# Kernel tuning notes

Measured on AMD Instinct MI355X. Metric: run time of the kernel, lower is better.

The kernel has to match this reference:

```python
import jax, jax.numpy as jnp
import numpy as np

N_NODES = 50000
N_EDGES = 800000
IN_DIM = 128
HID = 128
NUM_CLASSES = 2


def setup_inputs() -> dict:
    key = jax.random.key(0)
    ks = jax.random.split(key, 16)
    inp = {
        "adj_row": jax.random.randint(ks[0], (N_EDGES,), 0, N_NODES),
        "adj_col": jax.random.randint(ks[1], (N_EDGES,), 0, N_NODES),
        "adj_vals": jax.random.uniform(ks[2], (N_EDGES,), dtype=jnp.float32),
        "input_feature": jax.random.normal(ks[3], (N_NODES, IN_DIM), dtype=jnp.float32),
        "graph_indicator": jax.random.randint(ks[4], (N_NODES,), 0, 64),
        # GCN layer params (kaiming-uniform-ish init; zeros bias like the torch module)
        "W1": jax.random.uniform(ks[5], (IN_DIM, HID), jnp.float32, -1, 1) * np.sqrt(6.0 / IN_DIM),
        "b1": jnp.zeros((HID,), jnp.float32),
        "W2": jax.random.uniform(ks[6], (HID, HID), jnp.float32, -1, 1) * np.sqrt(6.0 / HID),
        "b2": jnp.zeros((HID,), jnp.float32),
        "W3": jax.random.uniform(ks[7], (HID, HID), jnp.float32, -1, 1) * np.sqrt(6.0 / HID),
        "b3": jnp.zeros((HID,), jnp.float32),
        # fc params (torch.nn.Linear default init range)
        "fcW1": jax.random.uniform(ks[8], (3 * HID, HID), jnp.float32, -1, 1) / np.sqrt(3 * HID),
        "fcb1": jax.random.uniform(ks[9], (HID,), jnp.float32, -1, 1) / np.sqrt(3 * HID),
        "fcW2": jax.random.uniform(ks[10], (HID, HID // 2), jnp.float32, -1, 1) / np.sqrt(HID),
        "fcb2": jax.random.uniform(ks[11], (HID // 2,), jnp.float32, -1, 1) / np.sqrt(HID),
        "fcW3": jax.random.uniform(ks[12], (HID // 2, NUM_CLASSES), jnp.float32, -1, 1) / np.sqrt(HID // 2),
        "fcb3": jax.random.uniform(ks[13], (NUM_CLASSES,), jnp.float32, -1, 1) / np.sqrt(HID // 2),
    }
    return inp


def _gcn_layer(row, col, vals, x, W, b, n_nodes):
    # support = X @ W  -> dense GEMM
    support = x @ W
    # sparse.mm(A, support): out[i] = sum_{e: row[e]=i} vals[e] * support[col[e]]
    msgs = support[col] * vals[:, None]  # [E, D] gather + scale
    agg = jax.ops.segment_sum(msgs, row, num_segments=n_nodes)
    return agg + b


def reference(adj_row, adj_col, adj_vals, input_feature, graph_indicator,
              W1, b1, W2, b2, W3, b3, fcW1, fcb1, fcW2, fcb2, fcW3, fcb3):
    n = input_feature.shape[0]
    g1 = jax.nn.relu(_gcn_layer(adj_row, adj_col, adj_vals, input_feature, W1, b1, n))
    g2 = jax.nn.relu(_gcn_layer(adj_row, adj_col, adj_vals, g1, W2, b2, n))
    g3 = jax.nn.relu(_gcn_layer(adj_row, adj_col, adj_vals, g2, W3, b3, n))
    feat = jnp.concatenate([g1, g2, g3], axis=1)  # [N, 3*HID]
    h = jax.nn.relu(feat @ fcW1 + fcb1)
    h = jax.nn.relu(h @ fcW2 + fcb2)
    logits = h @ fcW3 + fcb3
    return logits
```

## Files before the change

### kernel.cpp

```cpp
#include <hip/hip_runtime.h>
#include <hip/hip_bf16.h>

#define N_NODES 50000
#define N_EDGES 800000
#define NBK 391
#define BCAP 2560
#define PADSLACK 896

static inline int cdiv(int a, int b) { return (a + b - 1) / b; }

typedef __attribute__((ext_vector_type(8))) short short8;
typedef __attribute__((ext_vector_type(4))) float f32x4;

__device__ __forceinline__ float b2f(unsigned short u) {
    union { unsigned int i; float f; } c;
    c.i = ((unsigned int)u) << 16;
    return c.f;
}
__device__ __forceinline__ unsigned short f2bb(float f) {
    __hip_bfloat16 h = __float2bfloat16(f);
    return *(unsigned short*)&h;
}

__device__ __forceinline__ void pack_one(const float* __restrict__ W,
                                         __hip_bfloat16* __restrict__ out,
                                         int K, int N, int t) {
    int lane = t & 63;
    int kc = (t >> 6) % (K / 32);
    int nt = (t >> 6) / (K / 32);
    int kbase = kc * 32 + (lane >> 4) * 8;
    int col = nt * 16 + (lane & 15);
    __hip_bfloat16* dst = out + (size_t)t * 8;
#pragma unroll
    for (int j = 0; j < 8; ++j)
        dst[j] = __float2bfloat16(W[(size_t)(kbase + j) * N + col]);
}

__global__ __launch_bounds__(256)
void stage1_kernel(const int* __restrict__ row, const int* __restrict__ col,
                   const float* __restrict__ vals, int* __restrict__ bcursor,
                   int2* __restrict__ tmp, int E,
                   const float* __restrict__ x, __hip_bfloat16* __restrict__ support,
                   int M,
                   const float* __restrict__ W1, const float* __restrict__ W2,
                   const float* __restrict__ W3, const float* __restrict__ fcW1,
                   const float* __restrict__ fcW2,
                   __hip_bfloat16* __restrict__ pW2, __hip_bfloat16* __restrict__ pW3,
                   __hip_bfloat16* __restrict__ pfcW1, __hip_bfloat16* __restrict__ pfcW2) {
    __shared__ unsigned short As[64][136];
    __shared__ int hist[NBK];
    __shared__ int base[NBK];
    const int b = blockIdx.x;
    const int tid = threadIdx.x;

    if (b < 196) {
        const int CH = 4096;
        int e0 = b * CH;
        for (int i = tid; i < NBK; i += 256) hist[i] = 0;
        __syncthreads();
        for (int i = tid; i < CH; i += 256) {
            int e = e0 + i;
            if (e < E) atomicAdd(&hist[row[e] >> 7], 1);
        }
        __syncthreads();
        for (int i = tid; i < NBK; i += 256) {
            int c = hist[i];
            base[i] = (c > 0) ? (i * BCAP + atomicAdd(&bcursor[i], c)) : 0;
            hist[i] = 0;
        }
        __syncthreads();
        for (int i = tid; i < CH; i += 256) {
            int e = e0 + i;
            if (e < E) {
                int r = row[e];
                int bk = r >> 7;
                int rk = atomicAdd(&hist[bk], 1);
                tmp[base[bk] + rk] = make_int2(((r & 127) << 16) | col[e],
                                               __float_as_int(vals[e]));
            }
        }
        return;
    }

    if (b < 978) {
        const int wave = tid >> 6;
        const int lane = tid & 63;
        const int ln15 = lane & 15;
        const int quad = lane >> 4;
        const int m0 = (b - 196) * 64;

        short8 bfr[4][2];
#pragma unroll
        for (int kc = 0; kc < 4; ++kc)
#pragma unroll
            for (int h = 0; h < 2; ++h)
#pragma unroll
                for (int j = 0; j < 8; ++j)
                    bfr[kc][h][j] = (short)f2bb(
                        W1[(size_t)(kc * 32 + quad * 8 + j) * 128 + (wave * 2 + h) * 16 + ln15]);

#pragma unroll
        for (int i = 0; i < 4; ++i) {
            int idx = tid + i * 256;
            int r = idx >> 4;
            int c8 = (idx & 15) * 8;
            uint4 pk = {0, 0, 0, 0};
            if (m0 + r < M) {
                const float* src = &x[(size_t)(m0 + r) * 128 + c8];
                float4 a = *(const float4*)src;
                float4 bq = *(const float4*)(src + 4);
                pk.x = f2bb(a.x) | ((unsigned int)f2bb(a.y) << 16);
                pk.y = f2bb(a.z) | ((unsigned int)f2bb(a.w) << 16);
                pk.z = f2bb(bq.x) | ((unsigned int)f2bb(bq.y) << 16);
                pk.w = f2bb(bq.z) | ((unsigned int)f2bb(bq.w) << 16);
            }
            *(uint4*)&As[r][c8] = pk;
        }
        __syncthreads();

        f32x4 acc[4][2];
#pragma unroll
        for (int s = 0; s < 4; ++s)
#pragma unroll
            for (int h = 0; h < 2; ++h) acc[s][h] = (f32x4){0.f, 0.f, 0.f, 0.f};
#pragma unroll
        for (int kc = 0; kc < 4; ++kc) {
            short8 af[4];
#pragma unroll
            for (int s = 0; s < 4; ++s)
                af[s] = *(const short8*)&As[s * 16 + ln15][kc * 32 + quad * 8];
#pragma unroll
            for (int s = 0; s < 4; ++s)
#pragma unroll
                for (int h = 0; h < 2; ++h)
                    acc[s][h] = __builtin_amdgcn_mfma_f32_16x16x32_bf16(
                        af[s], bfr[kc][h], acc[s][h], 0, 0, 0);
        }
#pragma unroll
        for (int s = 0; s < 4; ++s)
#pragma unroll
            for (int h = 0; h < 2; ++h) {
                int cl = (wave * 2 + h) * 16 + ln15;
#pragma unroll
                for (int r = 0; r < 4; ++r) {
                    int rw = m0 + s * 16 + quad * 4 + r;
                    if (rw < M)
                        support[(size_t)rw * 128 + cl] = __float2bfloat16(acc[s][h][r]);
                }
            }
        return;
    }

    int pb = b - 978;
    if (pb < 8)       pack_one(W2,  pW2,  128, 128, pb * 256 + tid);
    else if (pb < 16) pack_one(W3,  pW3,  128, 128, (pb - 8) * 256 + tid);
    else if (pb < 40) pack_one(fcW1, pfcW1, 384, 128, (pb - 16) * 256 + tid);
    else              pack_one(fcW2, pfcW2, 128, 64, (pb - 40) * 256 + tid);
}

__global__ __launch_bounds__(256)
void binB_kernel(const int2* __restrict__ tmp, const int* __restrict__ bcursor,
                 int2* __restrict__ rowrange, int2* __restrict__ epack, int N) {
    int b = blockIdx.x;
    int r0 = b << 7;
    int nr = N - r0; if (nr > 128) nr = 128;
    __shared__ int cnt[128];
    __shared__ int cur[128];
    __shared__ int rpos[128];
    __shared__ int red[256];
    int t = threadIdx.x;
    int partial = 0;
    for (int i = t; i < b; i += 256) partial += bcursor[i];
    red[t] = partial;
    if (t < 128) cnt[t] = 0;
    __syncthreads();
    for (int off = 128; off > 0; off >>= 1) {
        if (t < off) red[t] += red[t + off];
        __syncthreads();
    }
    int slab = b * BCAP;
    int send = slab + bcursor[b];
    for (int i = slab + t; i < send; i += 256)
        atomicAdd(&cnt[tmp[i].x >> 16], 1);
    __syncthreads();
    int rcnt = (t < 128) ? cnt[t] : 0;
    int pc = (rcnt + 7) & ~7;
    if (t < 128) cur[t] = pc;
    __syncthreads();
    for (int off = 1; off < 128; off <<= 1) {
        int u = (t >= off && t < 128) ? cur[t - off] : 0;
        __syncthreads();
        if (t < 128) cur[t] += u;
        __syncthreads();
    }
    int obase = red[0] + b * PADSLACK;
    if (t < 128) {
        int pos = obase + cur[t] - pc;
        rpos[t] = pos;
        cur[t] = pos;
        if (t < nr) rowrange[r0 + t] = make_int2(pos, pos + pc);
    }
    __syncthreads();
    for (int i = slab + t; i < send; i += 256) {
        int2 v = tmp[i];
        int rl = v.x >> 16;
        int c = v.x & 0xffff;
        int pos = atomicAdd(&cur[rl], 1);
        epack[pos] = make_int2(c, v.y);
    }
    if (t < 128) {
        int rc = rcnt;
        int pos = rpos[t];
#pragma unroll 1
        for (int i = pos + rc; i < pos + pc; ++i)
            epack[i] = make_int2(0, 0);
    }
}

__device__ __forceinline__ void accum8(float* acc, long long e, uint4 u) {
    float f = __int_as_float((int)(e >> 32));
    acc[0] += f * b2f((unsigned short)(u.x & 0xffff));
    acc[1] += f * b2f((unsigned short)(u.x >> 16));
    acc[2] += f * b2f((unsigned short)(u.y & 0xffff));
    acc[3] += f * b2f((unsigned short)(u.y >> 16));
    acc[4] += f * b2f((unsigned short)(u.z & 0xffff));
    acc[5] += f * b2f((unsigned short)(u.z >> 16));
    acc[6] += f * b2f((unsigned short)(u.w & 0xffff));
    acc[7] += f * b2f((unsigned short)(u.w >> 16));
}

__device__ __forceinline__ void agg_node(const long long* __restrict__ ep,
                                         const __hip_bfloat16* __restrict__ support,
                                         int p, int end, int g, int j, float* acc) {
#pragma unroll
    for (int k = 0; k < 8; ++k) acc[k] = 0.f;
    long long e0 = 0, e1 = 0;
    uint4 u0 = {0, 0, 0, 0}, u1 = {0, 0, 0, 0};
    bool have = false;
    if (p < end) {
        e0 = ep[p + g];
        e1 = ep[p + 4 + g];
        u0 = *(const uint4*)&support[(size_t)(unsigned int)(e0 & 0xffffffffu) * 128 + j * 8];
        u1 = *(const uint4*)&support[(size_t)(unsigned int)(e1 & 0xffffffffu) * 128 + j * 8];
        p += 8;
        have = true;
    }
    while (p < end) {
        long long f0 = ep[p + g];
        long long f1 = ep[p + 4 + g];
        uint4 w0 = *(const uint4*)&support[(size_t)(unsigned int)(f0 & 0xffffffffu) * 128 + j * 8];
        uint4 w1 = *(const uint4*)&support[(size_t)(unsigned int)(f1 & 0xffffffffu) * 128 + j * 8];
        accum8(acc, e0, u0);
        accum8(acc, e1, u1);
        e0 = f0; u0 = w0; e1 = f1; u1 = w1;
        p += 8;
    }
    if (have) {
        accum8(acc, e0, u0);
        accum8(acc, e1, u1);
    }
#pragma unroll
    for (int k = 0; k < 8; ++k) {
        acc[k] += __shfl_xor(acc[k], 16);
        acc[k] += __shfl_xor(acc[k], 32);
    }
}

__global__ __launch_bounds__(256, 8)
void spmm_gemm_kernel(const int2* __restrict__ rowrange,
                      const int2* __restrict__ epack,
                      const __hip_bfloat16* __restrict__ support,
                      const float* __restrict__ bias,
                      __hip_bfloat16* __restrict__ gout,
                      const __hip_bfloat16* __restrict__ pW,
                      __hip_bfloat16* __restrict__ Cout,
                      int N) {
    __shared__ unsigned short As[16][136];
    const int tid = threadIdx.x;
    const int wv = tid >> 6;
    const int l = tid & 63;
    const int g = l >> 4;
    const int j = l & 15;
    const int m0 = blockIdx.x * 16;
    const long long* ep = (const long long*)epack;
    float4 b0 = *(const float4*)&bias[j * 8];
    float4 b1 = *(const float4*)&bias[j * 8 + 4];

    for (int i = 0; i < 4; ++i) {
        int node = m0 + wv * 4 + i;
        if (node < N) {
            int2 rr = rowrange[node];
            float acc[8];
            agg_node(ep, support, rr.x, rr.y, g, j, acc);
            if (g == 0) {
                unsigned int q0 = (unsigned int)f2bb(fmaxf(acc[0] + b0.x, 0.f))
                                | ((unsigned int)f2bb(fmaxf(acc[1] + b0.y, 0.f)) << 16);
                unsigned int q1 = (unsigned int)f2bb(fmaxf(acc[2] + b0.z, 0.f))
                                | ((unsigned int)f2bb(fmaxf(acc[3] + b0.w, 0.f)) << 16);
                unsigned int q2 = (unsigned int)f2bb(fmaxf(acc[4] + b1.x, 0.f))
                                | ((unsigned int)f2bb(fmaxf(acc[5] + b1.y, 0.f)) << 16);
                unsigned int q3 = (unsigned int)f2bb(fmaxf(acc[6] + b1.z, 0.f))
                                | ((unsigned int)f2bb(fmaxf(acc[7] + b1.w, 0.f)) << 16);
                uint4 st = {q0, q1, q2, q3};
                *(uint4*)&As[wv * 4 + i][j * 8] = st;
                *(uint4*)&gout[(size_t)node * 384 + j * 8] = st;
            }
        } else if (g == 0) {
            *(uint4*)&As[wv * 4 + i][j * 8] = (uint4){0, 0, 0, 0};
        }
    }
    __syncthreads();

    const int ln15 = l & 15;
    const int quad = l >> 4;
    f32x4 acc2[2];
    acc2[0] = (f32x4){0.f, 0.f, 0.f, 0.f};
    acc2[1] = (f32x4){0.f, 0.f, 0.f, 0.f};
#pragma unroll
    for (int kc = 0; kc < 4; ++kc) {
        short8 af = *(const short8*)&As[ln15][kc * 32 + quad * 8];
#pragma unroll
        for (int h = 0; h < 2; ++h) {
            int nt = wv * 2 + h;
            short8 bf = *(const short8*)&pW[((size_t)(nt * 4 + kc) * 64 + l) * 8];
            acc2[h] = __builtin_amdgcn_mfma_f32_16x16x32_bf16(af, bf, acc2[h], 0, 0, 0);
        }
    }
#pragma unroll
    for (int h = 0; h < 2; ++h) {
        int cl = (wv * 2 + h) * 16 + ln15;
#pragma unroll
        for (int r = 0; r < 4; ++r) {
            int rw = m0 + quad * 4 + r;
            if (rw < N)
                Cout[(size_t)rw * 128 + cl] = __float2bfloat16(acc2[h][r]);
        }
    }
}

__global__ __launch_bounds__(256, 8)
void spmm_fc_kernel(const int2* __restrict__ rowrange,
                    const int2* __restrict__ epack,
                    const __hip_bfloat16* __restrict__ support,
                    const float* __restrict__ bias,
                    const __hip_bfloat16* __restrict__ featb,
                    const __hip_bfloat16* __restrict__ pfcW1,
                    const float* __restrict__ fcb1,
                    const __hip_bfloat16* __restrict__ pfcW2,
                    const float* __restrict__ fcb2,
                    const float* __restrict__ fcW3, const float* __restrict__ fcb3,
                    float* __restrict__ out, int N) {
    __shared__ unsigned short As[16][136];
    __shared__ float w3s[128];
    __shared__ float b3s[2];
    const int tid = threadIdx.x;
    const int wv = tid >> 6;
    const int l = tid & 63;
    const int g = l >> 4;
    const int j = l & 15;
    const int m0 = blockIdx.x * 16;
    const long long* ep = (const long long*)epack;
    if (tid < 128) w3s[tid] = fcW3[tid];
    if (tid < 2) b3s[tid] = fcb3[tid];
    float4 b0 = *(const float4*)&bias[j * 8];
    float4 b1 = *(const float4*)&bias[j * 8 + 4];

    for (int i = 0; i < 4; ++i) {
        int node = m0 + wv * 4 + i;
        if (node < N) {
            int2 rr = rowrange[node];
            float acc[8];
            agg_node(ep, support, rr.x, rr.y, g, j, acc);
            if (g == 0) {
                unsigned int q0 = (unsigned int)f2bb(fmaxf(acc[0] + b0.x, 0.f))
                                | ((unsigned int)f2bb(fmaxf(acc[1] + b0.y, 0.f)) << 16);
                unsigned int q1 = (unsigned int)f2bb(fmaxf(acc[2] + b0.z, 0.f))
                                | ((unsigned int)f2bb(fmaxf(acc[3] + b0.w, 0.f)) << 16);
                unsigned int q2 = (unsigned int)f2bb(fmaxf(acc[4] + b1.x, 0.f))
                                | ((unsigned int)f2bb(fmaxf(acc[5] + b1.y, 0.f)) << 16);
                unsigned int q3 = (unsigned int)f2bb(fmaxf(acc[6] + b1.z, 0.f))
                                | ((unsigned int)f2bb(fmaxf(acc[7] + b1.w, 0.f)) << 16);
                uint4 st = {q0, q1, q2, q3};
                *(uint4*)&As[wv * 4 + i][j * 8] = st;
            }
        } else if (g == 0) {
            *(uint4*)&As[wv * 4 + i][j * 8] = (uint4){0, 0, 0, 0};
        }
    }
    __syncthreads();

    const int ln15 = l & 15;
    const int quad = l >> 4;
    f32x4 acc[2];
    acc[0] = (f32x4){0.f, 0.f, 0.f, 0.f};
    acc[1] = (f32x4){0.f, 0.f, 0.f, 0.f};
#pragma unroll
    for (int step = 0; step < 3; ++step) {
        const int kb = (step == 0) ? 2 : (step - 1);
        if (step != 0) {
            __syncthreads();
            int r = tid >> 4;
            int c8 = (tid & 15) * 8;
            *(uint4*)&As[r][c8] =
                *(const uint4*)&featb[(size_t)(m0 + r) * 384 + kb * 128 + c8];
            __syncthreads();
        }
#pragma unroll
        for (int kc = 0; kc < 4; ++kc) {
            short8 af = *(const short8*)&As[ln15][kc * 32 + quad * 8];
            int kcg = kb * 4 + kc;
#pragma unroll
            for (int h = 0; h < 2; ++h) {
                int nt = wv * 2 + h;
                short8 bf = *(const short8*)&pfcW1[((size_t)(nt * 12 + kcg) * 64 + l) * 8];
                acc[h] = __builtin_amdgcn_mfma_f32_16x16x32_bf16(af, bf, acc[h], 0, 0, 0);
            }
        }
    }
    __syncthreads();
#pragma unroll
    for (int h = 0; h < 2; ++h) {
        int col = (wv * 2 + h) * 16 + ln15;
        float bv = fcb1[col];
#pragma unroll
        for (int r = 0; r < 4; ++r)
            As[quad * 4 + r][col] = f2bb(fmaxf(acc[h][r] + bv, 0.f));
    }
    __syncthreads();

    f32x4 acc2 = (f32x4){0.f, 0.f, 0.f, 0.f};
#pragma unroll
    for (int kc = 0; kc < 4; ++kc) {
        short8 af = *(const short8*)&As[ln15][kc * 32 + quad * 8];
        short8 bfw = *(const short8*)&pfcW2[((size_t)(wv * 4 + kc) * 64 + l) * 8];
        acc2 = __builtin_amdgcn_mfma_f32_16x16x32_bf16(af, bfw, acc2, 0, 0, 0);
    }
    __syncthreads();
    {
        int col2 = wv * 16 + ln15;
        float bv = fcb2[col2];
#pragma unroll
        for (int r = 0; r < 4; ++r)
            As[quad * 4 + r][col2] = f2bb(fmaxf(acc2[r] + bv, 0.f));
    }
    __syncthreads();

    if (tid < 32) {
        int row = tid >> 1, cls = tid & 1;
        int grow = m0 + row;
        if (grow < N) {
            float a = b3s[cls];
#pragma unroll
            for (int k = 0; k < 64; ++k)
                a += b2f(As[row][k]) * w3s[k * 2 + cls];
            out[(size_t)grow * 2 + cls] = a;
        }
    }
}

extern "C" void kernel_launch(void* const* d_in, const int* in_sizes, int n_in,
                              void* d_out, int out_size, void* d_ws, size_t ws_size,
                              hipStream_t stream) {
    const int*   adj_row  = (const int*)d_in[0];
    const int*   adj_col  = (const int*)d_in[1];
    const float* adj_vals = (const float*)d_in[2];
    const float* x        = (const float*)d_in[3];
    const float* W1   = (const float*)d_in[5];
    const float* b1   = (const float*)d_in[6];
    const float* W2   = (const float*)d_in[7];
    const float* b2   = (const float*)d_in[8];
    const float* W3   = (const float*)d_in[9];
    const float* b3   = (const float*)d_in[10];
    const float* fcW1 = (const float*)d_in[11];
    const float* fcb1 = (const float*)d_in[12];
    const float* fcW2 = (const float*)d_in[13];
    const float* fcb2 = (const float*)d_in[14];
    const float* fcW3 = (const float*)d_in[15];
    const float* fcb3 = (const float*)d_in[16];
    float* out = (float*)d_out;

    const int N = N_NODES, E = N_EDGES;
    const int Mpad = 50048;
    const int EPAD = E + NBK * PADSLACK + 64;

    char* p = (char*)d_ws;
    auto alloc = [&](size_t bytes) {
        char* q = p;
        p += (bytes + 255) & ~(size_t)255;
        return q;
    };
    __hip_bfloat16* featb    = (__hip_bfloat16*)alloc((size_t)Mpad * 384 * 2);
    __hip_bfloat16* supportb = (__hip_bfloat16*)alloc((size_t)Mpad * 128 * 2);
    __hip_bfloat16* supportc = (__hip_bfloat16*)alloc((size_t)Mpad * 128 * 2);
    __hip_bfloat16* pW2   = (__hip_bfloat16*)alloc(16384 * 2);
    __hip_bfloat16* pW3   = (__hip_bfloat16*)alloc(16384 * 2);
    __hip_bfloat16* pfcW1 = (__hip_bfloat16*)alloc(49152 * 2);
    __hip_bfloat16* pfcW2 = (__hip_bfloat16*)alloc(8192 * 2);
    int2*  rowrange  = (int2*)alloc((size_t)(N + 1) * 8);
    int*   bcursor   = (int*)alloc((size_t)NBK * 4);
    int2*  epack     = (int2*)alloc((size_t)EPAD * 8);
    int2*  tmp       = (int2*)alloc((size_t)NBK * BCAP * 8);

    hipMemsetAsync(bcursor, 0, (size_t)NBK * 4, stream);
    stage1_kernel<<<1022, 256, 0, stream>>>(adj_row, adj_col, adj_vals, bcursor, tmp, E,
                                            x, supportb, N,
                                            W1, W2, W3, fcW1, fcW2,
                                            pW2, pW3, pfcW1, pfcW2);
    binB_kernel<<<NBK, 256, 0, stream>>>(tmp, bcursor, rowrange, epack, N);

    const int fgrid = cdiv(N, 16);

    spmm_gemm_kernel<<<fgrid, 256, 0, stream>>>(rowrange, epack, supportb, b1,
                                                featb + 0, pW2, supportc, N);
    spmm_gemm_kernel<<<fgrid, 256, 0, stream>>>(rowrange, epack, supportc, b2,
                                                featb + 128, pW3, supportb, N);
    spmm_fc_kernel<<<fgrid, 256, 0, stream>>>(rowrange, epack, supportb, b3,
                                              featb, pfcW1, fcb1, pfcW2, fcb2,
                                              fcW3, fcb3, out, N);
}
```

Baseline: 250.4 us.

## Build CSR via global histogram/scan/scatter and interleave two-node aggregation

Result: slower. 345.6 us (+38.0%).

```diff
diff --git a/kernel.cpp b/kernel.cpp
--- a/kernel.cpp
+++ b/kernel.cpp
@@ -3,9 +3,6 @@
 
 #define N_NODES 50000
 #define N_EDGES 800000
-#define NBK 391
-#define BCAP 2560
-#define PADSLACK 896
 
 static inline int cdiv(int a, int b) { return (a + b - 1) / b; }
 
@@ -37,9 +34,7 @@
 }
 
 __global__ __launch_bounds__(256)
-void stage1_kernel(const int* __restrict__ row, const int* __restrict__ col,
-                   const float* __restrict__ vals, int* __restrict__ bcursor,
-                   int2* __restrict__ tmp, int E,
+void stage1_kernel(const int* __restrict__ row, int* __restrict__ hist, int E,
                    const float* __restrict__ x, __hip_bfloat16* __restrict__ support,
                    int M,
                    const float* __restrict__ W1, const float* __restrict__ W2,
@@ -48,36 +43,16 @@
                    __hip_bfloat16* __restrict__ pW2, __hip_bfloat16* __restrict__ pW3,
                    __hip_bfloat16* __restrict__ pfcW1, __hip_bfloat16* __restrict__ pfcW2) {
     __shared__ unsigned short As[64][136];
-    __shared__ int hist[NBK];
-    __shared__ int base[NBK];
     const int b = blockIdx.x;
     const int tid = threadIdx.x;
 
     if (b < 196) {
         const int CH = 4096;
         int e0 = b * CH;
-        for (int i = tid; i < NBK; i += 256) hist[i] = 0;
-        __syncthreads();
+#pragma unroll 4
         for (int i = tid; i < CH; i += 256) {
             int e = e0 + i;
-            if (e < E) atomicAdd(&hist[row[e] >> 7], 1);
-        }
-        __syncthreads();
-        for (int i = tid; i < NBK; i += 256) {
-            int c = hist[i];
-            base[i] = (c > 0) ? (i * BCAP + atomicAdd(&bcursor[i], c)) : 0;
-            hist[i] = 0;
-        }
-        __syncthreads();
-        for (int i = tid; i < CH; i += 256) {
-            int e = e0 + i;
-            if (e < E) {
-                int r = row[e];
-                int bk = r >> 7;
-                int rk = atomicAdd(&hist[bk], 1);
-                tmp[base[bk] + rk] = make_int2(((r & 127) << 16) | col[e],
-                                               __float_as_int(vals[e]));
-            }
+            if (e < E) atomicAdd(&hist[row[e]], 1);
         }
         return;
     }
@@ -158,62 +133,44 @@
     else              pack_one(fcW2, pfcW2, 128, 64, (pb - 40) * 256 + tid);
 }
 
+__global__ __launch_bounds__(128)
+void scan_kernel(int* __restrict__ hist, int* __restrict__ gtotal,
+                 int2* __restrict__ rowrange, int2* __restrict__ epack, int N) {
+    __shared__ int s[128];
+    __shared__ int sbase;
+    const int t = threadIdx.x;
+    const int r = blockIdx.x * 128 + t;
+    int cnt = (r < N) ? hist[r] : 0;
+    int pc = (cnt + 7) & ~7;
+    s[t] = pc;
+    __syncthreads();
+    for (int off = 1; off < 128; off <<= 1) {
+        int u = (t >= off) ? s[t - off] : 0;
+        __syncthreads();
+        s[t] += u;
+        __syncthreads();
+    }
+    if (t == 127) sbase = atomicAdd(gtotal, s[127]);
+    __syncthreads();
+    int pos = sbase + s[t] - pc;
+    if (r < N) {
+        rowrange[r] = make_int2(pos, pos + pc);
+        hist[r] = pos;
+#pragma unroll 1
+        for (int i = pos + cnt; i < pos + pc; ++i)
+            epack[i] = make_int2(0, 0);
+    }
+}
+
 __global__ __launch_bounds__(256)
-void binB_kernel(const int2* __restrict__ tmp, const int* __restrict__ bcursor,
-                 int2* __restrict__ rowrange, int2* __restrict__ epack, int N) {
-    int b = blockIdx.x;
-    int r0 = b << 7;
-    int nr = N - r0; if (nr > 128) nr = 128;
-    __shared__ int cnt[128];
-    __shared__ int cur[128];
-    __shared__ int rpos[128];
-    __shared__ int red[256];
-    int t = threadIdx.x;
-    int partial = 0;
-    for (int i = t; i < b; i += 256) partial += bcursor[i];
-    red[t] = partial;
-    if (t < 128) cnt[t] = 0;
-    __syncthreads();
-    for (int off = 128; off > 0; off >>= 1) {
-        if (t < off) red[t] += red[t + off];
-        __syncthreads();
-    }
-    int slab = b * BCAP;
-    int send = slab + bcursor[b];
-    for (int i = slab + t; i < send; i += 256)
-        atomicAdd(&cnt[tmp[i].x >> 16], 1);
-    __syncthreads();
-    int rcnt = (t < 128) ? cnt[t] : 0;
-    int pc = (rcnt + 7) & ~7;
-    if (t < 128) cur[t] = pc;
-    __syncthreads();
-    for (int off = 1; off < 128; off <<= 1) {
-        int u = (t >= off && t < 128) ? cur[t - off] : 0;
-        __syncthreads();
-        if (t < 128) cur[t] += u;
-        __syncthreads();
-    }
-    int obase = red[0] + b * PADSLACK;
-    if (t < 128) {
-        int pos = obase + cur[t] - pc;
-        rpos[t] = pos;
-        cur[t] = pos;
-        if (t < nr) rowrange[r0 + t] = make_int2(pos, pos + pc);
-    }
-    __syncthreads();
-    for (int i = slab + t; i < send; i += 256) {
-        int2 v = tmp[i];
-        int rl = v.x >> 16;
-        int c = v.x & 0xffff;
-        int pos = atomicAdd(&cur[rl], 1);
-        epack[pos] = make_int2(c, v.y);
-    }
-    if (t < 128) {
-        int rc = rcnt;
-        int pos = rpos[t];
-#pragma unroll 1
-        for (int i = pos + rc; i < pos + pc; ++i)
-            epack[i] = make_int2(0, 0);
+void scatter_kernel(const int* __restrict__ row, const int* __restrict__ col,
+                    const float* __restrict__ vals, int* __restrict__ cur,
+                    int2* __restrict__ epack, int E) {
+    int e = blockIdx.x * 256 + threadIdx.x;
+    if (e < E) {
+        int r = row[e];
+        int pos = atomicAdd(&cur[r], 1);
+        epack[pos] = make_int2(col[e], __float_as_int(vals[e]));
     }
 }
 
@@ -229,44 +186,80 @@
     acc[7] += f * b2f((unsigned short)(u.w >> 16));
 }
 
-__device__ __forceinline__ void agg_node(const long long* __restrict__ ep,
-                                         const __hip_bfloat16* __restrict__ support,
-                                         int p, int end, int g, int j, float* acc) {
-#pragma unroll
-    for (int k = 0; k < 8; ++k) acc[k] = 0.f;
-    long long e0 = 0, e1 = 0;
-    uint4 u0 = {0, 0, 0, 0}, u1 = {0, 0, 0, 0};
-    bool have = false;
-    if (p < end) {
-        e0 = ep[p + g];
-        e1 = ep[p + 4 + g];
-        u0 = *(const uint4*)&support[(size_t)(unsigned int)(e0 & 0xffffffffu) * 128 + j * 8];
-        u1 = *(const uint4*)&support[(size_t)(unsigned int)(e1 & 0xffffffffu) * 128 + j * 8];
-        p += 8;
-        have = true;
-    }
-    while (p < end) {
-        long long f0 = ep[p + g];
-        long long f1 = ep[p + 4 + g];
-        uint4 w0 = *(const uint4*)&support[(size_t)(unsigned int)(f0 & 0xffffffffu) * 128 + j * 8];
-        uint4 w1 = *(const uint4*)&support[(size_t)(unsigned int)(f1 & 0xffffffffu) * 128 + j * 8];
-        accum8(acc, e0, u0);
-        accum8(acc, e1, u1);
-        e0 = f0; u0 = w0; e1 = f1; u1 = w1;
-        p += 8;
-    }
-    if (have) {
-        accum8(acc, e0, u0);
-        accum8(acc, e1, u1);
-    }
+__device__ __forceinline__ void agg_node2(const long long* __restrict__ ep,
+                                          const __hip_bfloat16* __restrict__ support,
+                                          int p0, int end0, int p1, int end1,
+                                          int g, int j, float* acc0, float* acc1) {
+#pragma unroll
+    for (int k = 0; k < 8; ++k) { acc0[k] = 0.f; acc1[k] = 0.f; }
+    long long ea0 = 0, ea1 = 0, eb0 = 0, eb1 = 0;
+    uint4 ua0 = {0,0,0,0}, ua1 = {0,0,0,0}, ub0 = {0,0,0,0}, ub1 = {0,0,0,0};
+    const bool hA = (p0 < end0), hB = (p1 < end1);
+    if (hA) {
+        ea0 = ep[p0 + g]; ea1 = ep[p0 + 4 + g];
+        ua0 = *(const uint4*)&support[(size_t)(unsigned int)(ea0 & 0xffffffffu) * 128 + j * 8];
+        ua1 = *(const uint4*)&support[(size_t)(unsigned int)(ea1 & 0xffffffffu) * 128 + j * 8];
+        p0 += 8;
+    }
+    if (hB) {
+        eb0 = ep[p1 + g]; eb1 = ep[p1 + 4 + g];
+        ub0 = *(const uint4*)&support[(size_t)(unsigned int)(eb0 & 0xffffffffu) * 128 + j * 8];
+        ub1 = *(const uint4*)&support[(size_t)(unsigned int)(eb1 & 0xffffffffu) * 128 + j * 8];
+        p1 += 8;
+    }
+    while (p0 < end0 && p1 < end1) {
+        long long fa0 = ep[p0 + g], fa1 = ep[p0 + 4 + g];
+        long long fb0 = ep[p1 + g], fb1 = ep[p1 + 4 + g];
+        uint4 wa0 = *(const uint4*)&support[(size_t)(unsigned int)(fa0 & 0xffffffffu) * 128 + j * 8];
+        uint4 wa1 = *(const uint4*)&support[(size_t)(unsigned int)(fa1 & 0xffffffffu) * 128 + j * 8];
+        uint4 wb0 = *(const uint4*)&support[(size_t)(unsigned int)(fb0 & 0xffffffffu) * 128 + j * 8];
+        uint4 wb1 = *(const uint4*)&support[(size_t)(unsigned int)(fb1 & 0xffffffffu) * 128 + j * 8];
+        accum8(acc0, ea0, ua0); accum8(acc0, ea1, ua1);
+        accum8(acc1, eb0, ub0); accum8(acc1, eb1, ub1);
+        ea0 = fa0; ua0 = wa0; ea1 = fa1; ua1 = wa1;
+        eb0 = fb0; ub0 = wb0; eb1 = fb1; ub1 = wb1;
+        p0 += 8; p1 += 8;
+    }
+    while (p0 < end0) {
+        long long fa0 = ep[p0 + g], fa1 = ep[p0 + 4 + g];
+        uint4 wa0 = *(const uint4*)&support[(size_t)(unsigned int)(fa0 & 0xffffffffu) * 128 + j * 8];
+        uint4 wa1 = *(const uint4*)&support[(size_t)(unsigned int)(fa1 & 0xffffffffu) * 128 + j * 8];
+        accum8(acc0, ea0, ua0); accum8(acc0, ea1, ua1);
+        ea0 = fa0; ua0 = wa0; ea1 = fa1; ua1 = wa1;
+        p0 += 8;
+    }
+    while (p1 < end1) {
+        long long fb0 = ep[p1 + g], fb1 = ep[p1 + 4 + g];
+        uint4 wb0 = *(const uint4*)&support[(size_t)(unsigned int)(fb0 & 0xffffffffu) * 128 + j * 8];
+        uint4 wb1 = *(const uint4*)&support[(size_t)(unsigned int)(fb1 & 0xffffffffu) * 128 + j * 8];
+        accum8(acc1, eb0, ub0); accum8(acc1, eb1, ub1);
+        eb0 = fb0; ub0 = wb0; eb1 = fb1; ub1 = wb1;
+        p1 += 8;
+    }
+    if (hA) { accum8(acc0, ea0, ua0); accum8(acc0, ea1, ua1); }
+    if (hB) { accum8(acc1, eb0, ub0); accum8(acc1, eb1, ub1); }
 #pragma unroll
     for (int k = 0; k < 8; ++k) {
-        acc[k] += __shfl_xor(acc[k], 16);
-        acc[k] += __shfl_xor(acc[k], 32);
-    }
-}
-
-__global__ __launch_bounds__(256, 8)
+        acc0[k] += __shfl_xor(acc0[k], 16);
+        acc0[k] += __shfl_xor(acc0[k], 32);
+        acc1[k] += __shfl_xor(acc1[k], 16);
+        acc1[k] += __shfl_xor(acc1[k], 32);
+    }
+}
+
+__device__ __forceinline__ uint4 pack_row8(const float* acc, float4 b0, float4 b1) {
+    unsigned int q0 = (unsigned int)f2bb(fmaxf(acc[0] + b0.x, 0.f))
+                    | ((unsigned int)f2bb(fmaxf(acc[1] + b0.y, 0.f)) << 16);
+    unsigned int q1 = (unsigned int)f2bb(fmaxf(acc[2] + b0.z, 0.f))
+                    | ((unsigned int)f2bb(fmaxf(acc[3] + b0.w, 0.f)) << 16);
+    unsigned int q2 = (unsigned int)f2bb(fmaxf(acc[4] + b1.x, 0.f))
+                    | ((unsigned int)f2bb(fmaxf(acc[5] + b1.y, 0.f)) << 16);
+    unsigned int q3 = (unsigned int)f2bb(fmaxf(acc[6] + b1.z, 0.f))
+                    | ((unsigned int)f2bb(fmaxf(acc[7] + b1.w, 0.f)) << 16);
+    return (uint4){q0, q1, q2, q3};
+}
+
+__global__ __launch_bounds__(256, 6)
 void spmm_gemm_kernel(const int2* __restrict__ rowrange,
                       const int2* __restrict__ epack,
                       const __hip_bfloat16* __restrict__ support,
@@ -286,27 +279,20 @@
     float4 b0 = *(const float4*)&bias[j * 8];
     float4 b1 = *(const float4*)&bias[j * 8 + 4];
 
-    for (int i = 0; i < 4; ++i) {
-        int node = m0 + wv * 4 + i;
-        if (node < N) {
-            int2 rr = rowrange[node];
-            float acc[8];
-            agg_node(ep, support, rr.x, rr.y, g, j, acc);
-            if (g == 0) {
-                unsigned int q0 = (unsigned int)f2bb(fmaxf(acc[0] + b0.x, 0.f))
-                                | ((unsigned int)f2bb(fmaxf(acc[1] + b0.y, 0.f)) << 16);
-                unsigned int q1 = (unsigned int)f2bb(fmaxf(acc[2] + b0.z, 0.f))
-                                | ((unsigned int)f2bb(fmaxf(acc[3] + b0.w, 0.f)) << 16);
-                unsigned int q2 = (unsigned int)f2bb(fmaxf(acc[4] + b1.x, 0.f))
-                                | ((unsigned int)f2bb(fmaxf(acc[5] + b1.y, 0.f)) << 16);
-                unsigned int q3 = (unsigned int)f2bb(fmaxf(acc[6] + b1.z, 0.f))
-                                | ((unsigned int)f2bb(fmaxf(acc[7] + b1.w, 0.f)) << 16);
-                uint4 st = {q0, q1, q2, q3};
-                *(uint4*)&As[wv * 4 + i][j * 8] = st;
-                *(uint4*)&gout[(size_t)node * 384 + j * 8] = st;
-            }
-        } else if (g == 0) {
-            *(uint4*)&As[wv * 4 + i][j * 8] = (uint4){0, 0, 0, 0};
+#pragma unroll
+    for (int i = 0; i < 4; i += 2) {
+        int node0 = m0 + wv * 4 + i;
+        int2 r0 = rowrange[node0];
+        int2 r1 = rowrange[node0 + 1];
+        float acc0[8], acc1[8];
+        agg_node2(ep, support, r0.x, r0.y, r1.x, r1.y, g, j, acc0, acc1);
+        if (g == 0) {
+            uint4 s0 = pack_row8(acc0, b0, b1);
+            uint4 s1 = pack_row8(acc1, b0, b1);
+            *(uint4*)&As[wv * 4 + i][j * 8] = s0;
+            *(uint4*)&As[wv * 4 + i + 1][j * 8] = s1;
+            *(uint4*)&gout[(size_t)node0 * 384 + j * 8] = s0;
+            *(uint4*)&gout[(size_t)(node0 + 1) * 384 + j * 8] = s1;
         }
     }
     __syncthreads();
@@ -332,13 +318,12 @@
 #pragma unroll
         for (int r = 0; r < 4; ++r) {
             int rw = m0 + quad * 4 + r;
-            if (rw < N)
-                Cout[(size_t)rw * 128 + cl] = __float2bfloat16(acc2[h][r]);
-        }
-    }
-}
-
-__global__ __launch_bounds__(256, 8)
+            Cout[(size_t)rw * 128 + cl] = __float2bfloat16(acc2[h][r]);
+        }
+    }
+}
+
+__global__ __launch_bounds__(256, 6)
 void spmm_fc_kernel(const int2* __restrict__ rowrange,
                     const int2* __restrict__ epack,
                     const __hip_bfloat16* __restrict__ support,
@@ -365,26 +350,16 @@
     float4 b0 = *(const float4*)&bias[j * 8];
     float4 b1 = *(const float4*)&bias[j * 8 + 4];
 
-    for (int i = 0; i < 4; ++i) {
-        int node = m0 + wv * 4 + i;
-        if (node < N) {
-            int2 rr = rowrange[node];
-            float acc[8];
-            agg_node(ep, support, rr.x, rr.y, g, j, acc);
-            if (g == 0) {
-                unsigned int q0 = (unsigned int)f2bb(fmaxf(acc[0] + b0.x, 0.f))
-                                | ((unsigned int)f2bb(fmaxf(acc[1] + b0.y, 0.f)) << 16);
-                unsigned int q1 = (unsigned int)f2bb(fmaxf(acc[2] + b0.z, 0.f))
-                                | ((unsigned int)f2bb(fmaxf(acc[3] + b0.w, 0.f)) << 16);
-                unsigned int q2 = (unsigned int)f2bb(fmaxf(acc[4] + b1.x, 0.f))
-                                | ((unsigned int)f2bb(fmaxf(acc[5] + b1.y, 0.f)) << 16);
-                unsigned int q3 = (unsigned int)f2bb(fmaxf(acc[6] + b1.z, 0.f))
-                                | ((unsigned int)f2bb(fmaxf(acc[7] + b1.w, 0.f)) << 16);
-                uint4 st = {q0, q1, q2, q3};
-                *(uint4*)&As[wv * 4 + i][j * 8] = st;
-            }
-        } else if (g == 0) {
-            *(uint4*)&As[wv * 4 + i][j * 8] = (uint4){0, 0, 0, 0};
+#pragma unroll
+    for (int i = 0; i < 4; i += 2) {
+        int node0 = m0 + wv * 4 + i;
+        int2 r0 = rowrange[node0];
+        int2 r1 = rowrange[node0 + 1];
+        float acc0[8], acc1[8];
+        agg_node2(ep, support, r0.x, r0.y, r1.x, r1.y, g, j, acc0, acc1);
+        if (g == 0) {
+            *(uint4*)&As[wv * 4 + i][j * 8] = pack_row8(acc0, b0, b1);
+            *(uint4*)&As[wv * 4 + i + 1][j * 8] = pack_row8(acc1, b0, b1);
         }
     }
     __syncthreads();
@@ -448,13 +423,11 @@
     if (tid < 32) {
         int row = tid >> 1, cls = tid & 1;
         int grow = m0 + row;
-        if (grow < N) {
-            float a = b3s[cls];
-#pragma unroll
-            for (int k = 0; k < 64; ++k)
-                a += b2f(As[row][k]) * w3s[k * 2 + cls];
-            out[(size_t)grow * 2 + cls] = a;
-        }
+        float a = b3s[cls];
+#pragma unroll
+        for (int k = 0; k < 64; ++k)
+            a += b2f(As[row][k]) * w3s[k * 2 + cls];
+        out[(size_t)grow * 2 + cls] = a;
     }
 }
 
@@ -481,7 +454,7 @@
 
     const int N = N_NODES, E = N_EDGES;
     const int Mpad = 50048;
-    const int EPAD = E + NBK * PADSLACK + 64;
+    const int EPAD = E + 7 * N_NODES + 64;
 
     char* p = (char*)d_ws;
     auto alloc = [&](size_t bytes) {
@@ -497,16 +470,17 @@
     __hip_bfloat16* pfcW1 = (__hip_bfloat16*)alloc(49152 * 2);
     __hip_bfloat16* pfcW2 = (__hip_bfloat16*)alloc(8192 * 2);
     int2*  rowrange  = (int2*)alloc((size_t)(N + 1) * 8);
-    int*   bcursor   = (int*)alloc((size_t)NBK * 4);
+    int*   hist      = (int*)alloc((size_t)(N + 1) * 4);
     int2*  epack     = (int2*)alloc((size_t)EPAD * 8);
-    int2*  tmp       = (int2*)alloc((size_t)NBK * BCAP * 8);
-
-    hipMemsetAsync(bcursor, 0, (size_t)NBK * 4, stream);
-    stage1_kernel<<<1022, 256, 0, stream>>>(adj_row, adj_col, adj_vals, bcursor, tmp, E,
+
+    hipMemsetAsync(hist, 0, (size_t)(N + 1) * 4, stream);
+    stage1_kernel<<<1022, 256, 0, stream>>>(adj_row, hist, E,
                                             x, supportb, N,
                                             W1, W2, W3, fcW1, fcW2,
                                             pW2, pW3, pfcW1, pfcW2);
-    binB_kernel<<<NBK, 256, 0, stream>>>(tmp, bcursor, rowrange, epack, N);
+    scan_kernel<<<cdiv(N, 128), 128, 0, stream>>>(hist, hist + N, rowrange, epack, N);
+    scatter_kernel<<<cdiv(E, 256), 256, 0, stream>>>(adj_row, adj_col, adj_vals, hist,
+                                                     epack, E);
 
     const int fgrid = cdiv(N, 16);
 
```
